# Kernel tuning notes

Measured on AMD Instinct MI355X. Metric: run time of the kernel, lower is better.

## Reference

```python
import jax, jax.numpy as jnp
import numpy as np

N_NODES = 100000
N_EDGES = 1600000
N_GRAPHS = 64
IN_DIM, HID, OUT_DIM = 64, 128, 32


def _glorot(key, shape):
    lim = float(np.sqrt(6.0 / (shape[0] + shape[1])))
    return jax.random.uniform(key, shape, jnp.float32, -lim, lim)


def setup_inputs() -> dict:
    key = jax.random.key(0)
    ks = jax.random.split(key, 20)
    x = jax.random.normal(ks[0], (N_NODES, IN_DIM), jnp.float32)
    edge_index = jax.random.randint(ks[1], (2, N_EDGES), 0, N_NODES, jnp.int64)
    batch = jnp.sort(jax.random.randint(ks[2], (N_NODES,), 0, N_GRAPHS, jnp.int64))
    d = {"x": x, "edge_index": edge_index, "batch": batch}
    dims = [(IN_DIM, HID), (HID, HID), (HID, HID), (HID, HID), (HID, OUT_DIM)]
    names = ["W1", "W2", "W3", "W4", "Wo"]
    bnames = ["b1", "b2", "b3", "b4", "bo"]
    for i, ((di, do), wn, bn) in enumerate(zip(dims, names, bnames)):
        d[wn] = _glorot(ks[3 + i], (di, do))
        d[bn] = jnp.zeros((do,), jnp.float32)
    # MLP: 32 -> 64 -> 8 -> 8  (hidden_dim//2, output_dim//2, output_dim//4)
    mdims = [(OUT_DIM, HID // 2), (HID // 2, OUT_DIM // 2), (OUT_DIM // 2, OUT_DIM // 4)]
    for i, (di, do) in enumerate(mdims):
        d[f"M{i+1}w"] = _glorot(ks[10 + i], (di, do))
        d[f"M{i+1}b"] = jnp.zeros((do,), jnp.float32)
    return d


def _gcn(x, src, dst, norm, W, b, n):
    h = x @ W                                    # [N, d_out] dense GEMM
    msg = h[src] * norm[:, None]                 # gather + normalize
    agg = jax.ops.segment_sum(msg, dst, num_segments=n)  # scatter-add
    return agg + b


def reference(x, edge_index, batch, W1, b1, W2, b2, W3, b3, W4, b4, Wo, bo,
              M1w, M1b, M2w, M2b, M3w, M3b):
    n = x.shape[0]
    # add self loops (PyG GCNConv default)
    loops = jnp.arange(n, dtype=edge_index.dtype)
    src = jnp.concatenate([edge_index[0], loops])
    dst = jnp.concatenate([edge_index[1], loops])
    # symmetric degree normalization: D^{-1/2} (A+I) D^{-1/2}
    deg = jax.ops.segment_sum(jnp.ones_like(src, dtype=x.dtype), dst, num_segments=n)
    dinv = jnp.where(deg > 0, jax.lax.rsqrt(deg), 0.0)
    norm = dinv[src] * dinv[dst]                 # [E+N]

    h = jax.nn.relu(_gcn(x, src, dst, norm, W1, b1, n))
    for W, b in ((W2, b2), (W3, b3), (W4, b4)):
        h = jax.nn.relu(_gcn(h, src, dst, norm, W, b, n))
    h = _gcn(h, src, dst, norm, Wo, bo, n)       # [N, 32]

    # global mean pool over graphs
    sums = jax.ops.segment_sum(h, batch, num_segments=N_GRAPHS)
    cnts = jax.ops.segment_sum(jnp.ones((n,), h.dtype), batch, num_segments=N_GRAPHS)
    g = sums / jnp.maximum(cnts, 1.0)[:, None]   # [G, 32]

    g = jax.nn.relu(g @ M1w + M1b)
    g = jax.nn.relu(g @ M2w + M2b)
    return g @ M3w + M3b                          # [G, 8]
```

## Files before the change

kernel.cpp:

```cpp
#include <hip/hip_runtime.h>


static constexpr int TPB = 256;
static constexpr int NBKT = 128;
static constexpr int NCHK = 256;

__device__ __forceinline__ float u2f(unsigned u) { return __uint_as_float(u); }

__device__ __forceinline__ unsigned bf2(float a, float b) {
    unsigned ua = __float_as_uint(a);
    unsigned ub = __float_as_uint(b);
    ua += 0x7FFFu + ((ua >> 16) & 1u);
    ub += 0x7FFFu + ((ub >> 16) & 1u);
    return (ua >> 16) | (ub & 0xFFFF0000u);
}

__global__ __launch_bounds__(256) void k_hist(const int* __restrict__ dst,
                                              int* __restrict__ histT, int E, int CS) {
    __shared__ int h[NBKT];
    int c = blockIdx.x, t = threadIdx.x;
    if (t < NBKT) h[t] = 0;
    __syncthreads();
    int e0 = c * CS, e1 = min(e0 + CS, E);
    for (int e = e0 + t; e < e1; e += 256)
        atomicAdd(&h[dst[e] >> 10], 1);
    __syncthreads();
    if (t < NBKT) histT[t * NCHK + c] = h[t];
}

__global__ __launch_bounds__(256) void k_scanS(const int* __restrict__ histT,
                                               int* __restrict__ stg) {
    constexpr int TOT = NBKT * NCHK;
    constexpr int PER = TOT / 256;
    __shared__ int s[256];
    int t = threadIdx.x;
    int base = t * PER;
    int sum = 0;
    for (int i = 0; i < PER; ++i) sum += histT[base + i];
    s[t] = sum;
    __syncthreads();
    for (int off = 1; off < 256; off <<= 1) {
        int add = (t >= off) ? s[t - off] : 0;
        __syncthreads();
        s[t] += add;
        __syncthreads();
    }
    int run = (t > 0) ? s[t - 1] : 0;
    for (int i = 0; i < PER; ++i) {
        stg[base + i] = run;
        run += histT[base + i];
    }
}

__global__ __launch_bounds__(256) void k_bucket(const int* __restrict__ src,
                                                const int* __restrict__ dst,
                                                const int* __restrict__ stg,
                                                unsigned* __restrict__ staging,
                                                int E, int CS) {
    __shared__ int cur[NBKT];
    int c = blockIdx.x, t = threadIdx.x;
    if (t < NBKT) cur[t] = stg[t * NCHK + c];
    __syncthreads();
    int e0 = c * CS, e1 = min(e0 + CS, E);
    for (int e = e0 + t; e < e1; e += 256) {
        int d = dst[e];
        int p = atomicAdd(&cur[d >> 10], 1);
        staging[p] = ((unsigned)src[e] << 10) | (unsigned)(d & 1023);
    }
}

__global__ __launch_bounds__(256) void k_deg(const unsigned* __restrict__ staging,
                                             const int* __restrict__ stg,
                                             int* __restrict__ cnt, int E, int n) {
    __shared__ int deg[1024];
    int r = blockIdx.x, t = threadIdx.x;
    for (int i = t; i < 1024; i += 256) deg[i] = 0;
    __syncthreads();
    int s0 = stg[r * NCHK];
    int s1 = (r == NBKT - 1) ? E : stg[(r + 1) * NCHK];
    for (int e = s0 + t; e < s1; e += 256)
        atomicAdd(&deg[staging[e] & 1023u], 1);
    __syncthreads();
    int b = r << 10;
    for (int i = t; i < 1024; i += 256)
        if (b + i < n) cnt[b + i] = deg[i];
}

__global__ void k_scanA(const int* __restrict__ cnt, int* __restrict__ rowptr,
                        int* __restrict__ bsum, int n) {
    __shared__ int s[TPB];
    int t = threadIdx.x;
    int i = blockIdx.x * TPB + t;
    s[t] = (i < n) ? cnt[i] : 0;
    __syncthreads();
    for (int off = 1; off < TPB; off <<= 1) {
        int add = (t >= off) ? s[t - off] : 0;
        __syncthreads();
        s[t] += add;
        __syncthreads();
    }
    if (i < n) rowptr[i + 1] = s[t];
    if (t == TPB - 1) bsum[blockIdx.x] = s[t];
}

__global__ void k_scanB(const int* __restrict__ bsum, int* __restrict__ bscan, int nb) {
    __shared__ int s[512];
    int t = threadIdx.x;
    s[t] = (t < nb) ? bsum[t] : 0;
    __syncthreads();
    for (int off = 1; off < 512; off <<= 1) {
        int add = (t >= off) ? s[t - off] : 0;
        __syncthreads();
        s[t] += add;
        __syncthreads();
    }
    if (t < nb) bscan[t] = (t > 0) ? s[t - 1] : 0;
}

__global__ void k_scanC(int* __restrict__ rowptr, const int* __restrict__ bscan,
                        const int* __restrict__ cnt, float* __restrict__ dinv, int n) {
    int i = blockIdx.x * blockDim.x + threadIdx.x;
    if (i >= n) return;
    rowptr[i + 1] += bscan[i >> 8];
    dinv[i] = rsqrtf((float)cnt[i] + 1.0f);
    if (i == 0) rowptr[0] = 0;
}

__global__ __launch_bounds__(256) void k_fill2(const unsigned* __restrict__ staging,
                                               const int* __restrict__ stg,
                                               const int* __restrict__ rowptr,
                                               int* __restrict__ csr, int E, int n) {
    __shared__ int cur[1024];
    int r = blockIdx.x, t = threadIdx.x;
    int b = r << 10;
    for (int i = t; i < 1024; i += 256)
        cur[i] = (b + i < n) ? rowptr[b + i] : 0;
    __syncthreads();
    int s0 = stg[r * NCHK];
    int s1 = (r == NBKT - 1) ? E : stg[(r + 1) * NCHK];
    for (int e = s0 + t; e < s1; e += 256) {
        unsigned sd = staging[e];
        int p = atomicAdd(&cur[sd & 1023u], 1);
        csr[p] = (int)(sd >> 10);
    }
}

__global__ void k_castx(const float* __restrict__ x, const float* __restrict__ dinv,
                        unsigned short* __restrict__ xs, int n) {
    int gid = blockIdx.x * blockDim.x + threadIdx.x;
    if (gid >= n * 8) return;
    int row = gid >> 3;
    float d = dinv[row];
    const float4* xp = (const float4*)x + (size_t)gid * 2;
    float4 a = xp[0], b = xp[1];
    uint4 o;
    o.x = bf2(a.x * d, a.y * d);
    o.y = bf2(a.z * d, a.w * d);
    o.z = bf2(b.x * d, b.y * d);
    o.w = bf2(b.z * d, b.w * d);
    ((uint4*)xs)[gid] = o;
}

template <int K, int OUT, int EPI>
__global__ __launch_bounds__(256) void k_gemm(const float* __restrict__ xin,
                                              const float* __restrict__ W,
                                              const float* __restrict__ dinv,
                                              const float* __restrict__ bias,
                                              void* __restrict__ outp, int n) {
    constexpr int CG = OUT / 16;
    constexpr int R = (OUT <= 32) ? 2 : 4;
    constexpr int ROWS = (256 / CG) * R;
    constexpr int KC = 32;
    constexpr int QS = OUT / 4;
    __shared__ float Wl[KC * OUT];

    int t = threadIdx.x;
    int cg = t % CG;
    int rl = t / CG;
    int r0 = blockIdx.x * ROWS + rl * R;

    float acc[R][16];
#pragma unroll
    for (int r = 0; r < R; ++r)
#pragma unroll
        for (int c = 0; c < 16; ++c) acc[r][c] = 0.f;

    const float4* W4 = (const float4*)W;
    const float4* xp[R];
    int rows[R];
    bool val[R];
#pragma unroll
    for (int r = 0; r < R; ++r) {
        rows[r] = r0 + r;
        val[r] = rows[r] < n;
        int rr = val[r] ? rows[r] : (n - 1);
        xp[r] = (const float4*)(xin + (size_t)rr * K);
    }

    for (int kc = 0; kc < K / KC; ++kc) {
        __syncthreads();
        for (int i = t; i < KC * OUT / 4; i += 256)
            ((float4*)Wl)[i] = W4[kc * (KC * OUT / 4) + i];
        __syncthreads();
#pragma unroll
        for (int k4 = 0; k4 < KC / 4; ++k4) {
            float4 xr[R];
#pragma unroll
            for (int r = 0; r < R; ++r) xr[r] = xp[r][kc * (KC / 4) + k4];
#pragma unroll
            for (int u = 0; u < 4; ++u) {
                float4 wq[4];
#pragma unroll
                for (int q = 0; q < 4; ++q)
                    wq[q] = *(const float4*)&Wl[(k4 * 4 + u) * OUT + cg * 4 + q * QS];
#pragma unroll
                for (int r = 0; r < R; ++r) {
                    float a = (u == 0) ? xr[r].x : (u == 1) ? xr[r].y
                                                : (u == 2) ? xr[r].z : xr[r].w;
#pragma unroll
                    for (int q = 0; q < 4; ++q) {
                        acc[r][q * 4 + 0] += a * wq[q].x;
                        acc[r][q * 4 + 1] += a * wq[q].y;
                        acc[r][q * 4 + 2] += a * wq[q].z;
                        acc[r][q * 4 + 3] += a * wq[q].w;
                    }
                }
            }
        }
    }

    if (EPI == 0) {
        unsigned short* ob = (unsigned short*)outp;
#pragma unroll
        for (int r = 0; r < R; ++r) {
            if (!val[r]) continue;
            float d = dinv[rows[r]];
#pragma unroll
            for (int q = 0; q < 4; ++q) {
                uint2 p;
                p.x = bf2(acc[r][q * 4 + 0] * d, acc[r][q * 4 + 1] * d);
                p.y = bf2(acc[r][q * 4 + 2] * d, acc[r][q * 4 + 3] * d);
                *(uint2*)(ob + (size_t)rows[r] * OUT + cg * 4 + q * QS) = p;
            }
        }
    } else {
        float* of = (float*)outp;
        float4 bq[4];
#pragma unroll
        for (int q = 0; q < 4; ++q) bq[q] = *(const float4*)&bias[cg * 4 + q * QS];
#pragma unroll
        for (int r = 0; r < R; ++r) {
            if (!val[r]) continue;
#pragma unroll
            for (int q = 0; q < 4; ++q) {
                float4 v;
                v.x = fmaxf(acc[r][q * 4 + 0] + bq[q].x, 0.f);
                v.y = fmaxf(acc[r][q * 4 + 1] + bq[q].y, 0.f);
                v.z = fmaxf(acc[r][q * 4 + 2] + bq[q].z, 0.f);
                v.w = fmaxf(acc[r][q * 4 + 3] + bq[q].w, 0.f);
                *(float4*)&of[(size_t)rows[r] * OUT + cg * 4 + q * QS] = v;
            }
        }
    }
}

__device__ __forceinline__ void addbf(float* acc, uint4 w) {
    acc[0] += u2f(w.x << 16); acc[1] += u2f(w.x & 0xFFFF0000u);
    acc[2] += u2f(w.y << 16); acc[3] += u2f(w.y & 0xFFFF0000u);
    acc[4] += u2f(w.z << 16); acc[5] += u2f(w.z & 0xFFFF0000u);
    acc[6] += u2f(w.w << 16); acc[7] += u2f(w.w & 0xFFFF0000u);
}

template <int D, bool RELU, bool HASBIAS>
__global__ __launch_bounds__(256) void k_gather_bf(const unsigned short* __restrict__ hsb,
                                                   const int* __restrict__ rowptr,
                                                   const int* __restrict__ csr,
                                                   const float* __restrict__ dinv,
                                                   const float* __restrict__ bias,
                                                   float* __restrict__ out, int n) {
    constexpr int TPN = D / 8;
    int gid = blockIdx.x * blockDim.x + threadIdx.x;
    int node = gid / TPN;
    if (node >= n) return;
    int c = gid % TPN;
    const uint4* hb = (const uint4*)hsb;

    float acc[8];
    {
        uint4 v = hb[(size_t)node * TPN + c];
        acc[0] = u2f(v.x << 16); acc[1] = u2f(v.x & 0xFFFF0000u);
        acc[2] = u2f(v.y << 16); acc[3] = u2f(v.y & 0xFFFF0000u);
        acc[4] = u2f(v.z << 16); acc[5] = u2f(v.z & 0xFFFF0000u);
        acc[6] = u2f(v.w << 16); acc[7] = u2f(v.w & 0xFFFF0000u);
    }
    int j0 = rowptr[node], j1 = rowptr[node + 1];
    int j = j0;
    for (; j + 3 < j1; j += 4) {
        int s0 = csr[j], s1 = csr[j + 1], s2 = csr[j + 2], s3 = csr[j + 3];
        uint4 w0 = hb[(size_t)s0 * TPN + c];
        uint4 w1 = hb[(size_t)s1 * TPN + c];
        uint4 w2 = hb[(size_t)s2 * TPN + c];
        uint4 w3 = hb[(size_t)s3 * TPN + c];
        addbf(acc, w0); addbf(acc, w1); addbf(acc, w2); addbf(acc, w3);
    }
    for (; j < j1; ++j) {
        uint4 w0 = hb[(size_t)csr[j] * TPN + c];
        addbf(acc, w0);
    }

    float di = dinv[node];
    float r[8];
    if (HASBIAS) {
        float4 b0 = *(const float4*)&bias[c * 8];
        float4 b1 = *(const float4*)&bias[c * 8 + 4];
        r[0] = di * acc[0] + b0.x; r[1] = di * acc[1] + b0.y;
        r[2] = di * acc[2] + b0.z; r[3] = di * acc[3] + b0.w;
        r[4] = di * acc[4] + b1.x; r[5] = di * acc[5] + b1.y;
        r[6] = di * acc[6] + b1.z; r[7] = di * acc[7] + b1.w;
    } else {
#pragma unroll
        for (int i = 0; i < 8; ++i) r[i] = di * acc[i];
    }
    if (RELU) {
#pragma unroll
        for (int i = 0; i < 8; ++i) r[i] = fmaxf(r[i], 0.f);
    }
    float4 o0 = {r[0], r[1], r[2], r[3]};
    float4 o1 = {r[4], r[5], r[6], r[7]};
    float4* op = (float4*)(out + (size_t)node * D + c * 8);
    op[0] = o0;
    op[1] = o1;
}

__global__ __launch_bounds__(256) void k_pool(const float* __restrict__ h,
                                              const int* __restrict__ batch,
                                              float* __restrict__ g, int n) {
    __shared__ int se[2];
    __shared__ float red[8][32];
    int gi = blockIdx.x;
    int t = threadIdx.x;
    if (t == 0) {
        int lo = 0, hi = n;
        while (lo < hi) { int m = (lo + hi) >> 1; if (batch[m] < gi) lo = m + 1; else hi = m; }
        se[0] = lo;
        lo = 0; hi = n;
        while (lo < hi) { int m = (lo + hi) >> 1; if (batch[m] < gi + 1) lo = m + 1; else hi = m; }
        se[1] = lo;
    }
    __syncthreads();
    int start = se[0], end = se[1];
    int col = t & 31, sub = t >> 5;
    float acc = 0.f;
    for (int i = start + sub; i < end; i += 8)
        acc += h[(size_t)i * 32 + col];
    red[sub][col] = acc;
    __syncthreads();
    if (t < 32) {
        float s = 0.f;
#pragma unroll
        for (int q = 0; q < 8; ++q) s += red[q][t];
        float c = (float)(end - start);
        g[gi * 32 + t] = s / fmaxf(c, 1.0f);
    }
}

template <int K, int O, bool RELU>
__global__ void k_mlp(const float* __restrict__ in, const float* __restrict__ W,
                      const float* __restrict__ b, float* __restrict__ out, int G) {
    int gid = blockIdx.x * blockDim.x + threadIdx.x;
    if (gid >= G * O) return;
    int g = gid / O, j = gid % O;
    float s = b[j];
    for (int k = 0; k < K; ++k) s += in[g * K + k] * W[k * O + j];
    if (RELU) s = fmaxf(s, 0.f);
    out[gid] = s;
}

extern "C" void kernel_launch(void* const* d_in, const int* in_sizes, int n_in,
                              void* d_out, int out_size, void* d_ws, size_t ws_size,
                              hipStream_t stream) {
    const float* x    = (const float*)d_in[0];
    const int*   ei   = (const int*)d_in[1];
    const int*   batch= (const int*)d_in[2];
    const float* W1 = (const float*)d_in[3];  const float* b1 = (const float*)d_in[4];
    const float* W2 = (const float*)d_in[5];  const float* b2 = (const float*)d_in[6];
    const float* W3 = (const float*)d_in[7];  const float* b3 = (const float*)d_in[8];
    const float* W4 = (const float*)d_in[9];  const float* b4 = (const float*)d_in[10];
    const float* Wo = (const float*)d_in[11]; const float* bo = (const float*)d_in[12];
    const float* M1w = (const float*)d_in[13]; const float* M1b = (const float*)d_in[14];
    const float* M2w = (const float*)d_in[15]; const float* M2b = (const float*)d_in[16];
    const float* M3w = (const float*)d_in[17]; const float* M3b = (const float*)d_in[18];

    const int N = in_sizes[0] / 64;
    const int E = in_sizes[1] / 2;
    const int G = out_size / 8;
    const int* src  = ei;
    const int* dstp = ei + E;

    char* w = (char*)d_ws;
    float* A   = (float*)w;
    unsigned short* xs = (unsigned short*)w;
    w += (size_t)N * 128 * 4;
    float* agg = (float*)w;
    unsigned short* hsb = (unsigned short*)w;
    w += (size_t)N * 128 * 2;
    int*      csr     = (int*)w;      w += (size_t)E * 4;
    unsigned* staging = (unsigned*)w; w += (size_t)E * 4;
    int*      histT   = (int*)w;      w += NBKT * NCHK * 4;
    int*      stg     = (int*)w;      w += NBKT * NCHK * 4;
    int*      cnt     = (int*)w;      w += (size_t)N * 4;
    int*      rowptr  = (int*)w;      w += (size_t)(N + 4) * 4;
    int*      bsum    = (int*)w;      w += 4096;
    int*      bscan   = (int*)w;      w += 4096;
    float*    dinv    = (float*)w;    w += (size_t)N * 4;
    float*    gp      = (float*)w;    w += 64 * 32 * 4;
    float*    m1      = (float*)w;    w += 64 * 64 * 4;
    float*    m2      = (float*)w;    w += 64 * 16 * 4;

    const int NB = (N + TPB - 1) / TPB;
    const int CS = (E + NCHK - 1) / NCHK;

    k_hist<<<NCHK, 256, 0, stream>>>(dstp, histT, E, CS);
    k_scanS<<<1, 256, 0, stream>>>(histT, stg);
    k_bucket<<<NCHK, 256, 0, stream>>>(src, dstp, stg, staging, E, CS);
    k_deg<<<NBKT, 256, 0, stream>>>(staging, stg, cnt, E, N);
    k_scanA<<<NB, TPB, 0, stream>>>(cnt, rowptr, bsum, N);
    k_scanB<<<1, 512, 0, stream>>>(bsum, bscan, NB);
    k_scanC<<<NB, TPB, 0, stream>>>(rowptr, bscan, cnt, dinv, N);
    k_fill2<<<NBKT, 256, 0, stream>>>(staging, stg, rowptr, csr, E, N);

    k_castx<<<(N * 8 + 255) / 256, 256, 0, stream>>>(x, dinv, xs, N);
    k_gather_bf<64, false, false><<<(N * 8 + 255) / 256, 256, 0, stream>>>(
        xs, rowptr, csr, dinv, nullptr, agg, N);
    k_gemm<64, 128, 1><<<(N + 127) / 128, 256, 0, stream>>>(agg, W1, nullptr, b1, A, N);

    k_gemm<128, 128, 0><<<(N + 127) / 128, 256, 0, stream>>>(A, W2, dinv, nullptr, hsb, N);
    k_gather_bf<128, true, true><<<(N * 16 + 255) / 256, 256, 0, stream>>>(
        hsb, rowptr, csr, dinv, b2, A, N);
    k_gemm<128, 128, 0><<<(N + 127) / 128, 256, 0, stream>>>(A, W3, dinv, nullptr, hsb, N);
    k_gather_bf<128, true, true><<<(N * 16 + 255) / 256, 256, 0, stream>>>(
        hsb, rowptr, csr, dinv, b3, A, N);
    k_gemm<128, 128, 0><<<(N + 127) / 128, 256, 0, stream>>>(A, W4, dinv, nullptr, hsb, N);
    k_gather_bf<128, true, true><<<(N * 16 + 255) / 256, 256, 0, stream>>>(
        hsb, rowptr, csr, dinv, b4, A, N);

    k_gemm<128, 32, 0><<<(N + 255) / 256, 256, 0, stream>>>(A, Wo, dinv, nullptr, hsb, N);
    k_gather_bf<32, false, true><<<(N * 4 + 255) / 256, 256, 0, stream>>>(
        hsb, rowptr, csr, dinv, bo, A, N);

    k_pool<<<G, 256, 0, stream>>>(A, batch, gp, N);
    k_mlp<32, 64, true><<<(G * 64 + 255) / 256, 256, 0, stream>>>(gp, M1w, M1b, m1, G);
    k_mlp<64, 16, true><<<(G * 16 + 255) / 256, 256, 0, stream>>>(m1, M2w, M2b, m2, G);
    k_mlp<16, 8, false><<<(G * 8 + 255) / 256, 256, 0, stream>>>(m2, M3w, M3b, (float*)d_out, G);
}
```

Baseline: 770.7 us.

## Replace FP32 SIMT GEMMs with bf16 MFMA using split-weight hi/lo and bf16 activations

```diff
diff --git a/kernel.cpp b/kernel.cpp
--- a/kernel.cpp
+++ b/kernel.cpp
@@ -5,7 +5,16 @@
 static constexpr int NBKT = 128;
 static constexpr int NCHK = 256;
 
+using f32x4  = __attribute__((ext_vector_type(4))) float;
+using bf16x8 = __attribute__((ext_vector_type(8))) short;
+
 __device__ __forceinline__ float u2f(unsigned u) { return __uint_as_float(u); }
+
+__device__ __forceinline__ unsigned short bf1(float a) {
+    unsigned u = __float_as_uint(a);
+    u += 0x7FFFu + ((u >> 16) & 1u);
+    return (unsigned short)(u >> 16);
+}
 
 __device__ __forceinline__ unsigned bf2(float a, float b) {
     unsigned ua = __float_as_uint(a);
@@ -161,104 +170,113 @@
     ((uint4*)xs)[gid] = o;
 }
 
+__global__ void k_prepw(const float* __restrict__ W1, const float* __restrict__ W2,
+                        const float* __restrict__ W3, const float* __restrict__ W4,
+                        const float* __restrict__ Wo,
+                        unsigned short* __restrict__ wt1, unsigned short* __restrict__ wt2,
+                        unsigned short* __restrict__ wt3, unsigned short* __restrict__ wt4,
+                        unsigned short* __restrict__ wto) {
+    int b = blockIdx.x, k = threadIdx.x;
+    const float* W; unsigned short* wt; int K, OUT, nn;
+    if (b < 128)      { W = W1; wt = wt1; K = 64;  OUT = 128; nn = b; }
+    else if (b < 256) { W = W2; wt = wt2; K = 128; OUT = 128; nn = b - 128; }
+    else if (b < 384) { W = W3; wt = wt3; K = 128; OUT = 128; nn = b - 256; }
+    else if (b < 512) { W = W4; wt = wt4; K = 128; OUT = 128; nn = b - 384; }
+    else              { W = Wo; wt = wto; K = 128; OUT = 32;  nn = b - 512; }
+    if (nn >= OUT || k >= K) return;
+    float v = W[(size_t)k * OUT + nn];
+    unsigned short hi = bf1(v);
+    float fhi = u2f((unsigned)hi << 16);
+    unsigned short lo = bf1(v - fhi);
+    wt[nn * K + k] = hi;
+    wt[OUT * K + nn * K + k] = lo;
+}
+
 template <int K, int OUT, int EPI>
-__global__ __launch_bounds__(256) void k_gemm(const float* __restrict__ xin,
-                                              const float* __restrict__ W,
-                                              const float* __restrict__ dinv,
-                                              const float* __restrict__ bias,
-                                              void* __restrict__ outp, int n) {
-    constexpr int CG = OUT / 16;
-    constexpr int R = (OUT <= 32) ? 2 : 4;
-    constexpr int ROWS = (256 / CG) * R;
-    constexpr int KC = 32;
-    constexpr int QS = OUT / 4;
-    __shared__ float Wl[KC * OUT];
+__global__ __launch_bounds__(256) void k_gemm_mfma(
+    const unsigned short* __restrict__ Ain,
+    const unsigned short* __restrict__ WT,
+    const float* __restrict__ dinv,
+    const float* __restrict__ bias,
+    unsigned short* __restrict__ out, int n) {
+    constexpr int NT = OUT / 16;
+    constexpr int KT = K / 32;
+    constexpr int CH = K / 8;
+    __shared__ __align__(16) unsigned short Wl[2 * OUT * K];
 
     int t = threadIdx.x;
-    int cg = t % CG;
-    int rl = t / CG;
-    int r0 = blockIdx.x * ROWS + rl * R;
-
-    float acc[R][16];
-#pragma unroll
-    for (int r = 0; r < R; ++r)
-#pragma unroll
-        for (int c = 0; c < 16; ++c) acc[r][c] = 0.f;
-
-    const float4* W4 = (const float4*)W;
-    const float4* xp[R];
-    int rows[R];
-    bool val[R];
-#pragma unroll
-    for (int r = 0; r < R; ++r) {
-        rows[r] = r0 + r;
-        val[r] = rows[r] < n;
-        int rr = val[r] ? rows[r] : (n - 1);
-        xp[r] = (const float4*)(xin + (size_t)rr * K);
-    }
-
-    for (int kc = 0; kc < K / KC; ++kc) {
-        __syncthreads();
-        for (int i = t; i < KC * OUT / 4; i += 256)
-            ((float4*)Wl)[i] = W4[kc * (KC * OUT / 4) + i];
-        __syncthreads();
-#pragma unroll
-        for (int k4 = 0; k4 < KC / 4; ++k4) {
-            float4 xr[R];
-#pragma unroll
-            for (int r = 0; r < R; ++r) xr[r] = xp[r][kc * (KC / 4) + k4];
-#pragma unroll
-            for (int u = 0; u < 4; ++u) {
-                float4 wq[4];
-#pragma unroll
-                for (int q = 0; q < 4; ++q)
-                    wq[q] = *(const float4*)&Wl[(k4 * 4 + u) * OUT + cg * 4 + q * QS];
-#pragma unroll
-                for (int r = 0; r < R; ++r) {
-                    float a = (u == 0) ? xr[r].x : (u == 1) ? xr[r].y
-                                                : (u == 2) ? xr[r].z : xr[r].w;
-#pragma unroll
-                    for (int q = 0; q < 4; ++q) {
-                        acc[r][q * 4 + 0] += a * wq[q].x;
-                        acc[r][q * 4 + 1] += a * wq[q].y;
-                        acc[r][q * 4 + 2] += a * wq[q].z;
-                        acc[r][q * 4 + 3] += a * wq[q].w;
-                    }
-                }
+    {
+        const uint4* wg = (const uint4*)WT;
+        uint4* wl = (uint4*)Wl;
+        for (int i = t; i < 2 * OUT * CH; i += 256) {
+            int m = i / (OUT * CH);
+            int r = i - m * (OUT * CH);
+            int nn = r / CH, g = r - nn * CH;
+            wl[m * OUT * CH + nn * CH + (g ^ (nn & 7))] = wg[i];
+        }
+    }
+
+    int wid = t >> 6, lane = t & 63;
+    int lr = lane & 15, lg = lane >> 4;
+    int mbase = blockIdx.x * 128 + wid * 32;
+
+    bf16x8 a[2][KT];
+#pragma unroll
+    for (int mt = 0; mt < 2; ++mt) {
+        int row = mbase + mt * 16 + lr;
+        row = row < n ? row : n - 1;
+        const bf16x8* ap = (const bf16x8*)(Ain + (size_t)row * K);
+#pragma unroll
+        for (int kt = 0; kt < KT; ++kt)
+            a[mt][kt] = ap[kt * 4 + lg];
+    }
+
+    __syncthreads();
+
+    f32x4 acc[2][NT] = {};
+#pragma unroll
+    for (int nt = 0; nt < NT; ++nt) {
+        int nn = nt * 16 + lr;
+        int swz = nn & 7;
+        int rowoff = nn * K;
+#pragma unroll
+        for (int kt = 0; kt < KT; ++kt) {
+            int g = kt * 4 + lg;
+            int off = rowoff + ((g ^ swz) * 8);
+            bf16x8 bhi = *(const bf16x8*)&Wl[off];
+            bf16x8 blo = *(const bf16x8*)&Wl[OUT * K + off];
+#pragma unroll
+            for (int mt = 0; mt < 2; ++mt) {
+                acc[mt][nt] = __builtin_amdgcn_mfma_f32_16x16x32_bf16(
+                    a[mt][kt], bhi, acc[mt][nt], 0, 0, 0);
+                acc[mt][nt] = __builtin_amdgcn_mfma_f32_16x16x32_bf16(
+                    a[mt][kt], blo, acc[mt][nt], 0, 0, 0);
             }
         }
     }
 
-    if (EPI == 0) {
-        unsigned short* ob = (unsigned short*)outp;
-#pragma unroll
-        for (int r = 0; r < R; ++r) {
-            if (!val[r]) continue;
-            float d = dinv[rows[r]];
-#pragma unroll
-            for (int q = 0; q < 4; ++q) {
-                uint2 p;
-                p.x = bf2(acc[r][q * 4 + 0] * d, acc[r][q * 4 + 1] * d);
-                p.y = bf2(acc[r][q * 4 + 2] * d, acc[r][q * 4 + 3] * d);
-                *(uint2*)(ob + (size_t)rows[r] * OUT + cg * 4 + q * QS) = p;
-            }
+#pragma unroll
+    for (int mt = 0; mt < 2; ++mt) {
+        int rbase = mbase + mt * 16 + lg * 4;
+        float dv[4];
+        if (EPI == 0) {
+#pragma unroll
+            for (int r = 0; r < 4; ++r)
+                dv[r] = (rbase + r < n) ? dinv[rbase + r] : 0.f;
         }
-    } else {
-        float* of = (float*)outp;
-        float4 bq[4];
-#pragma unroll
-        for (int q = 0; q < 4; ++q) bq[q] = *(const float4*)&bias[cg * 4 + q * QS];
-#pragma unroll
-        for (int r = 0; r < R; ++r) {
-            if (!val[r]) continue;
-#pragma unroll
-            for (int q = 0; q < 4; ++q) {
-                float4 v;
-                v.x = fmaxf(acc[r][q * 4 + 0] + bq[q].x, 0.f);
-                v.y = fmaxf(acc[r][q * 4 + 1] + bq[q].y, 0.f);
-                v.z = fmaxf(acc[r][q * 4 + 2] + bq[q].z, 0.f);
-                v.w = fmaxf(acc[r][q * 4 + 3] + bq[q].w, 0.f);
-                *(float4*)&of[(size_t)rows[r] * OUT + cg * 4 + q * QS] = v;
+#pragma unroll
+        for (int nt = 0; nt < NT; ++nt) {
+            int col = nt * 16 + lr;
+            float bb = (EPI == 1) ? bias[col] : 0.f;
+#pragma unroll
+            for (int r = 0; r < 4; ++r) {
+                int row = rbase + r;
+                if (row < n) {
+                    float v = acc[mt][nt][r];
+                    if (EPI == 0) v *= dv[r];
+                    else v = fmaxf(v + bb, 0.f);
+                    out[(size_t)row * OUT + col] = bf1(v);
+                }
             }
         }
     }
@@ -271,13 +289,13 @@
     acc[6] += u2f(w.w << 16); acc[7] += u2f(w.w & 0xFFFF0000u);
 }
 
-template <int D, bool RELU, bool HASBIAS>
+template <int D, bool RELU, bool HASBIAS, bool OUTBF>
 __global__ __launch_bounds__(256) void k_gather_bf(const unsigned short* __restrict__ hsb,
                                                    const int* __restrict__ rowptr,
                                                    const int* __restrict__ csr,
                                                    const float* __restrict__ dinv,
                                                    const float* __restrict__ bias,
-                                                   float* __restrict__ out, int n) {
+                                                   void* __restrict__ outp, int n) {
     constexpr int TPN = D / 8;
     int gid = blockIdx.x * blockDim.x + threadIdx.x;
     int node = gid / TPN;
@@ -325,11 +343,18 @@
 #pragma unroll
         for (int i = 0; i < 8; ++i) r[i] = fmaxf(r[i], 0.f);
     }
-    float4 o0 = {r[0], r[1], r[2], r[3]};
-    float4 o1 = {r[4], r[5], r[6], r[7]};
-    float4* op = (float4*)(out + (size_t)node * D + c * 8);
-    op[0] = o0;
-    op[1] = o1;
+    if (OUTBF) {
+        uint4 o;
+        o.x = bf2(r[0], r[1]); o.y = bf2(r[2], r[3]);
+        o.z = bf2(r[4], r[5]); o.w = bf2(r[6], r[7]);
+        ((uint4*)outp)[(size_t)node * TPN + c] = o;
+    } else {
+        float4 o0 = {r[0], r[1], r[2], r[3]};
+        float4 o1 = {r[4], r[5], r[6], r[7]};
+        float4* op = (float4*)outp + (size_t)node * TPN * 2 + c * 2;
+        op[0] = o0;
+        op[1] = o1;
+    }
 }
 
 __global__ __launch_bounds__(256) void k_pool(const float* __restrict__ h,
@@ -398,12 +423,9 @@
     const int* dstp = ei + E;
 
     char* w = (char*)d_ws;
-    float* A   = (float*)w;
-    unsigned short* xs = (unsigned short*)w;
-    w += (size_t)N * 128 * 4;
-    float* agg = (float*)w;
-    unsigned short* hsb = (unsigned short*)w;
-    w += (size_t)N * 128 * 2;
+    unsigned short* buf1 = (unsigned short*)w; w += (size_t)N * 128 * 2;
+    unsigned short* buf2 = (unsigned short*)w; w += (size_t)N * 128 * 2;
+    unsigned short* hsb  = (unsigned short*)w; w += (size_t)N * 128 * 2;
     int*      csr     = (int*)w;      w += (size_t)E * 4;
     unsigned* staging = (unsigned*)w; w += (size_t)E * 4;
     int*      histT   = (int*)w;      w += NBKT * NCHK * 4;
@@ -413,14 +435,21 @@
     int*      bsum    = (int*)w;      w += 4096;
     int*      bscan   = (int*)w;      w += 4096;
     float*    dinv    = (float*)w;    w += (size_t)N * 4;
+    unsigned short* wt1 = (unsigned short*)w; w += 2 * 128 * 64 * 2;
+    unsigned short* wt2 = (unsigned short*)w; w += 2 * 128 * 128 * 2;
+    unsigned short* wt3 = (unsigned short*)w; w += 2 * 128 * 128 * 2;
+    unsigned short* wt4 = (unsigned short*)w; w += 2 * 128 * 128 * 2;
+    unsigned short* wto = (unsigned short*)w; w += 2 * 32 * 128 * 2;
     float*    gp      = (float*)w;    w += 64 * 32 * 4;
     float*    m1      = (float*)w;    w += 64 * 64 * 4;
     float*    m2      = (float*)w;    w += 64 * 16 * 4;
 
     const int NB = (N + TPB - 1) / TPB;
     const int CS = (E + NCHK - 1) / NCHK;
+    const int GB = (N + 127) / 128;
 
     k_hist<<<NCHK, 256, 0, stream>>>(dstp, histT, E, CS);
+    k_prepw<<<544, 128, 0, stream>>>(W1, W2, W3, W4, Wo, wt1, wt2, wt3, wt4, wto);
     k_scanS<<<1, 256, 0, stream>>>(histT, stg);
     k_bucket<<<NCHK, 256, 0, stream>>>(src, dstp, stg, staging, E, CS);
     k_deg<<<NBKT, 256, 0, stream>>>(staging, stg, cnt, E, N);
@@ -429,26 +458,30 @@
     k_scanC<<<NB, TPB, 0, stream>>>(rowptr, bscan, cnt, dinv, N);
     k_fill2<<<NBKT, 256, 0, stream>>>(staging, stg, rowptr, csr, E, N);
 
+    unsigned short* agg = buf1;
+    unsigned short* xs  = buf2;
+
     k_castx<<<(N * 8 + 255) / 256, 256, 0, stream>>>(x, dinv, xs, N);
-    k_gather_bf<64, false, false><<<(N * 8 + 255) / 256, 256, 0, stream>>>(
+    k_gather_bf<64, false, false, true><<<(N * 8 + 255) / 256, 256, 0, stream>>>(
         xs, rowptr, csr, dinv, nullptr, agg, N);
-    k_gemm<64, 128, 1><<<(N + 127) / 128, 256, 0, stream>>>(agg, W1, nullptr, b1, A, N);
-
-    k_gemm<128, 128, 0><<<(N + 127) / 128, 256, 0, stream>>>(A, W2, dinv, nullptr, hsb, N);
-    k_gather_bf<128, true, true><<<(N * 16 + 255) / 256, 256, 0, stream>>>(
-        hsb, rowptr, csr, dinv, b2, A, N);
-    k_gemm<128, 128, 0><<<(N + 127) / 128, 256, 0, stream>>>(A, W3, dinv, nullptr, hsb, N);
-    k_gather_bf<128, true, true><<<(N * 16 + 255) / 256, 256, 0, stream>>>(
-        hsb, rowptr, csr, dinv, b3, A, N);
-    k_gemm<128, 128, 0><<<(N + 127) / 128, 256, 0, stream>>>(A, W4, dinv, nullptr, hsb, N);
-    k_gather_bf<128, true, true><<<(N * 16 + 255) / 256, 256, 0, stream>>>(
-        hsb, rowptr, csr, dinv, b4, A, N);
-
-    k_gemm<128, 32, 0><<<(N + 255) / 256, 256, 0, stream>>>(A, Wo, dinv, nullptr, hsb, N);
-    k_gather_bf<32, false, true><<<(N * 4 + 255) / 256, 256, 0, stream>>>(
-        hsb, rowptr, csr, dinv, bo, A, N);
-
-    k_pool<<<G, 256, 0, stream>>>(A, batch, gp, N);
+    k_gemm_mfma<64, 128, 1><<<GB, 256, 0, stream>>>(agg, wt1, nullptr, b1, buf2, N);
+
+    k_gemm_mfma<128, 128, 0><<<GB, 256, 0, stream>>>(buf2, wt2, dinv, nullptr, hsb, N);
+    k_gather_bf<128, true, true, true><<<(N * 16 + 255) / 256, 256, 0, stream>>>(
+        hsb, rowptr, csr, dinv, b2, buf1, N);
+    k_gemm_mfma<128, 128, 0><<<GB, 256, 0, stream>>>(buf1, wt3, dinv, nullptr, hsb, N);
+    k_gather_bf<128, true, true, true><<<(N * 16 + 255) / 256, 256, 0, stream>>>(
+        hsb, rowptr, csr, dinv, b3, buf2, N);
+    k_gemm_mfma<128, 128, 0><<<GB, 256, 0, stream>>>(buf2, wt4, dinv, nullptr, hsb, N);
+    k_gather_bf<128, true, true, true><<<(N * 16 + 255) / 256, 256, 0, stream>>>(
+        hsb, rowptr, csr, dinv, b4, buf1, N);
+
+    k_gemm_mfma<128, 32, 0><<<GB, 256, 0, stream>>>(buf1, wto, dinv, nullptr, hsb, N);
+    float* hout = (float*)buf2;
+    k_gather_bf<32, false, true, false><<<(N * 4 + 255) / 256, 256, 0, stream>>>(
+        hsb, rowptr, csr, dinv, bo, hout, N);
+
+    k_pool<<<G, 256, 0, stream>>>(hout, batch, gp, N);
     k_mlp<32, 64, true><<<(G * 64 + 255) / 256, 256, 0, stream>>>(gp, M1w, M1b, m1, G);
     k_mlp<64, 16, true><<<(G * 16 + 255) / 256, 256, 0, stream>>>(m1, M2w, M2b, m2, G);
     k_mlp<16, 8, false><<<(G * 8 + 255) / 256, 256, 0, stream>>>(m2, M3w, M3b, (float*)d_out, G);
```

Result: faster. 626.4 us (-18.7%).
